# Optimization experiments

Hardware: AMD Instinct MI355X
Metric: run time of the kernel (lower is better)

The kernel has to match this reference:

```python
import jax, jax.numpy as jnp
import numpy as np

# dims: batch, n_agent, action_dim, d_model, d_inner, d_state, d_conv, delta_rank, n_block, obs_dim
B, NA, AD = 128, 8, 16
DM, DI, DS, DC, DR, NB, OD = 512, 1024, 32, 4, 32, 4, 128


def _ln(x, scale):
    m = jnp.mean(x, axis=-1, keepdims=True)
    v = jnp.var(x, axis=-1, keepdims=True)
    return (x - m) / jnp.sqrt(v + 1e-5) * scale


def _mamba_step(u, W_in, cw, cb, W_x, W_dt, b_dt, A_log, D, W_out, h, buf):
    """Single recurrent Mamba step. u:[B,DM(in)], h:[B,DI,DS], buf:[B,DC,DI]."""
    xz = u @ W_in                                   # [B, 2*DI]
    x, z = xz[:, :DI], xz[:, DI:]
    # FIFO circular buffer push (roll + write last slot)
    buf = jnp.concatenate([buf[:, 1:], x[:, None, :]], axis=1)
    # depthwise causal conv evaluated at the newest position
    xc = jax.nn.silu(jnp.einsum('bkd,kd->bd', buf, cw) + cb)
    dbc = xc @ W_x                                  # [B, DR+2*DS]
    dt, Bm, Cm = dbc[:, :DR], dbc[:, DR:DR + DS], dbc[:, DR + DS:]
    delta = jax.nn.softplus(dt @ W_dt + b_dt)       # [B, DI]
    dA = jnp.exp(delta[:, :, None] * (-jnp.exp(A_log))[None])      # [B, DI, DS]
    h = dA * h + (delta * xc)[:, :, None] * Bm[:, None, :]
    y = jnp.einsum('bds,bs->bd', h, Cm) + D * xc
    return (y * jax.nn.silu(z)) @ W_out, h, buf


def _forward(obs_rep, obs, eps, W_embed, b_embed, W_obs, ln1_s, ln2_s, ln_out, W_head, log_std,
             in_proj_s, conv_w_s, conv_b_s, x_proj_s, dt_proj_s, dt_bias_s, A_log_s, D_s, out_proj_s,
             in_proj_c, conv_w_c, conv_b_c, x_proj_c, dt_proj_c, dt_bias_c, A_log_c, D_c, out_proj_c):
    h_s = [jnp.zeros((B, DI, DS))] * NB
    h_c = [jnp.zeros((B, DI, DS))] * NB
    bf_s = [jnp.zeros((B, DC, DI))] * NB
    bf_c = [jnp.zeros((B, DC, DI))] * NB
    std = jax.nn.softplus(log_std)
    log2pi = jnp.log(2.0 * jnp.pi)
    a_prev = jnp.zeros((B, AD))                     # shifted_action[:, 0]
    acts, raws, logs = [], [], []
    for i in range(NA):
        x = a_prev @ W_embed + b_embed
        ctx = obs_rep[:, i] + obs[:, i] @ W_obs
        for b in range(NB):
            o, h_s[b], bf_s[b] = _mamba_step(_ln(x, ln1_s[b]), in_proj_s[b], conv_w_s[b], conv_b_s[b],
                                             x_proj_s[b], dt_proj_s[b], dt_bias_s[b], A_log_s[b], D_s[b],
                                             out_proj_s[b], h_s[b], bf_s[b])
            x = x + o
            o, h_c[b], bf_c[b] = _mamba_step(_ln(x, ln2_s[b]) + ctx, in_proj_c[b], conv_w_c[b], conv_b_c[b],
                                             x_proj_c[b], dt_proj_c[b], dt_bias_c[b], A_log_c[b], D_c[b],
                                             out_proj_c[b], h_c[b], bf_c[b])
            x = x + o
        mean = _ln(x, ln_out) @ W_head
        raw = mean + std * eps[:, i]                # reparameterized Normal sample
        lp = -0.5 * jnp.sum(eps[:, i] ** 2, axis=-1) - jnp.sum(jnp.log(std)) - 0.5 * AD * log2pi
        lp = lp - jnp.sum(2.0 * (jnp.log(2.0) - raw - jax.nn.softplus(-2.0 * raw)), axis=-1)
        act = jnp.tanh(raw)
        acts.append(act); raws.append(raw); logs.append(lp)
        a_prev = act                                # feed sampled action forward
    return jnp.stack(acts, 1), jnp.stack(logs, 1), jnp.stack(raws, 1)


def setup_inputs() -> dict:
    key = jax.random.key(0)
    ks = jax.random.split(key, 8)
    def rn(k, shape, s=0.02):
        return jax.random.normal(k, shape) * s
    inp = {}
    inp['obs_rep'] = jax.random.normal(ks[0], (B, NA, DM))
    inp['obs'] = jax.random.normal(ks[1], (B, NA, OD))
    inp['eps'] = jax.random.normal(ks[2], (B, NA, AD))
    inp['W_embed'] = rn(ks[3], (AD, DM))
    inp['b_embed'] = jnp.zeros((DM,))
    inp['W_obs'] = rn(ks[4], (OD, DM))
    inp['ln1_s'] = jnp.ones((NB, DM))
    inp['ln2_s'] = jnp.ones((NB, DM))
    inp['ln_out'] = jnp.ones((DM,))
    inp['W_head'] = rn(ks[5], (DM, AD))
    inp['log_std'] = jnp.zeros((AD,)) - 0.5
    def mk(kbase):
        kk = jax.random.split(kbase, 8)
        dt_u = jax.random.uniform(kk[5], (NB, DI))
        dt = jnp.clip(jnp.exp(dt_u * (jnp.log(0.1) - jnp.log(1e-3)) + jnp.log(1e-3)), 1e-4)
        dt_bias = dt + jnp.log(-jnp.expm1(-dt))     # inverse-softplus init
        return dict(
            in_proj=rn(kk[0], (NB, DM, 2 * DI)),
            conv_w=rn(kk[1], (NB, DC, DI), 0.1),
            conv_b=jnp.zeros((NB, DI)),
            x_proj=rn(kk[2], (NB, DI, DR + 2 * DS)),
            dt_proj=rn(kk[3], (NB, DR, DI), DR ** -0.5),
            dt_bias=dt_bias,
            A_log=jnp.broadcast_to(jnp.log(jnp.arange(1, DS + 1, dtype=jnp.float32)), (NB, DI, DS)) + 0.0,
            D=jnp.ones((NB, DI)),
            out_proj=rn(kk[4], (NB, DI, DM)))
    ps, pc = mk(ks[6]), mk(ks[7])
    for n, v in ps.items():
        inp[n + '_s'] = v
    for n, v in pc.items():
        inp[n + '_c'] = v
    return inp


def reference(obs_rep, obs, eps, W_embed, b_embed, W_obs, ln1_s, ln2_s, ln_out, W_head, log_std,
              in_proj_s, conv_w_s, conv_b_s, x_proj_s, dt_proj_s, dt_bias_s, A_log_s, D_s, out_proj_s,
              in_proj_c, conv_w_c, conv_b_c, x_proj_c, dt_proj_c, dt_bias_c, A_log_c, D_c, out_proj_c):
    return _forward(obs_rep, obs, eps, W_embed, b_embed, W_obs, ln1_s, ln2_s, ln_out, W_head, log_std,
                    in_proj_s, conv_w_s, conv_b_s, x_proj_s, dt_proj_s, dt_bias_s, A_log_s, D_s, out_proj_s,
                    in_proj_c, conv_w_c, conv_b_c, x_proj_c, dt_proj_c, dt_bias_c, A_log_c, D_c, out_proj_c)
```

## Files before the change

kernel.cpp:

```cpp
#include <hip/hip_runtime.h>
#include <hip/hip_bf16.h>

#define B   128
#define NA  8
#define AD  16
#define DM  512
#define DI  1024
#define DS  32
#define DC  4
#define DR  32
#define NB  4
#define OD  128

typedef unsigned int uint32;
typedef _Float16 h2f __attribute__((ext_vector_type(2)));

__device__ __forceinline__ float sigmoidf_(float x){ return 1.0f/(1.0f+__expf(-x)); }
__device__ __forceinline__ float softplusf_(float x){ return fmaxf(x,0.0f)+log1pf(__expf(-fabsf(x))); }

__device__ __forceinline__ float dot2h(uint32 a, uint32 b, float c){
    union { uint32 u; h2f h; } ua, ub;
    ua.u = a; ub.u = b;
#if __has_builtin(__builtin_amdgcn_fdot2)
    return __builtin_amdgcn_fdot2(ua.h, ub.h, c, false);
#else
    return c + (float)ua.h.x*(float)ub.h.x + (float)ua.h.y*(float)ub.h.y;
#endif
}
__device__ __forceinline__ uint32 packh2(float a, float b){
    union { uint32 u; h2f h; } w;
    w.h.x = (_Float16)a; w.h.y = (_Float16)b;
    return w.u;
}
__device__ __forceinline__ float loh(uint32 u){
    union { uint32 uu; h2f h; } w; w.uu = u; return (float)w.h.x;
}
__device__ __forceinline__ float hih(uint32 u){
    union { uint32 uu; h2f h; } w; w.uu = u; return (float)w.h.y;
}


__global__ __launch_bounds__(256) void k_negA(const float* __restrict__ Als,
    const float* __restrict__ Alc, float* __restrict__ negA)
{
    int idx = blockIdx.x*256 + threadIdx.x;
    int bs = idx >> 15;
    int r  = idx & 32767;
    int nb = bs >> 1, st = bs & 1;
    const float* src = (st ? Alc : Als) + (size_t)nb*DI*DS + r;
    negA[idx] = -__expf(*src);
}

__global__ __launch_bounds__(256) void k_ctx(const float* __restrict__ obs_rep,
    const float* __restrict__ obs, const float* __restrict__ Wobs,
    float* __restrict__ ctx)
{
    int ib = blockIdx.x;
    int b = ib >> 3, i = ib & 7;
    __shared__ float orow[OD];
    int tid = threadIdx.x;
    if (tid < OD) orow[tid] = obs[(size_t)(b*NA+i)*OD + tid];
    __syncthreads();
    for (int m = tid; m < DM; m += 256){
        float acc = obs_rep[(size_t)(b*NA+i)*DM + m];
        for (int o = 0; o < OD; o++)
            acc += orow[o]*Wobs[o*DM + m];
        ctx[(size_t)(i*B + b)*DM + m] = acc;
    }
}

__global__ __launch_bounds__(256) void k_w1h(const float* __restrict__ Ws,
    const float* __restrict__ Wc, uint32* __restrict__ W1H)
{
    int idx = blockIdx.x*256 + threadIdx.x;
    int bs = idx >> 19;
    int r  = idx & 524287;
    int k2 = r >> 11, c = r & 2047;
    int nb = bs >> 1, st = bs & 1;
    const float* src = (st ? Wc : Ws) + (size_t)nb*1048576 + (size_t)(2*k2)*2048 + c;
    W1H[idx] = packh2(src[0], src[2048]);
}

__global__ __launch_bounds__(256) void k_woh(const float* __restrict__ Ws,
    const float* __restrict__ Wc, uint32* __restrict__ WoH)
{
    int idx = blockIdx.x*256 + threadIdx.x;
    int bs = idx >> 18;
    int r  = idx & 262143;
    int k2 = r >> 9, c = r & 511;
    int nb = bs >> 1, st = bs & 1;
    const float* src = (st ? Wc : Ws) + (size_t)nb*DI*DM + (size_t)(2*k2)*DM + c;
    WoH[idx] = packh2(src[0], src[DM]);
}

__global__ __launch_bounds__(256) void k_wxh(const float* __restrict__ Ws,
    const float* __restrict__ Wc, uint32* __restrict__ WxH)
{
    int idx = blockIdx.x*256 + threadIdx.x;
    int bs = idx / 49152;
    int r  = idx % 49152;
    int j  = r >> 9, k2 = r & 511;
    int nb = bs >> 1, st = bs & 1;
    const float* src = (st ? Wc : Ws) + (size_t)nb*DI*96 + (size_t)(2*k2)*96 + j;
    WxH[idx] = packh2(src[0], src[96]);
}

__global__ __launch_bounds__(256) void k_wdth(const float* __restrict__ Ws,
    const float* __restrict__ Wc, uint32* __restrict__ WdtH)
{
    int idx = blockIdx.x*256 + threadIdx.x;
    int bs = idx >> 14;
    int r  = idx & 16383;
    int r2 = r >> 10, d = r & 1023;
    int nb = bs >> 1, st = bs & 1;
    const float* src = (st ? Wc : Ws) + (size_t)nb*DR*DI + (size_t)(2*r2)*DI + d;
    WdtH[idx] = packh2(src[0], src[DI]);
}

__global__ __launch_bounds__(256) void k_init(const float* __restrict__ bemb,
    float* __restrict__ xb0, float* __restrict__ pP)
{
    int idx = blockIdx.x*256 + threadIdx.x;
    if (idx < B*DM) xb0[idx] = bemb[idx & (DM-1)];
    pP[idx] = 0.f;
}


struct SP {
    const uint32 *W1H, *WoH, *WxH, *WdtH;
    const float *negA, *ctxG;
    const float *cw_s, *cb_s, *dtb_s, *D_s;
    const float *cw_c, *cb_c, *dtb_c, *D_c;
    const float *ln1, *ln2;
    float *xcG, *szG, *xpP, *pP;
    uint32 *convrU, *hG;
};

__global__ __launch_bounds__(1024) void k_step1(SP P, const float* __restrict__ xin,
    float* __restrict__ xout, int i, int bs)
{
    int rg = blockIdx.x >> 3, cg = blockIdx.x & 7;
    int t = threadIdx.x;
    int st = bs & 1, nb = bs >> 1;
    const float* lns = (st ? P.ln2 : P.ln1) + (size_t)nb*DM;
    const float* cw  = (st ? P.cw_c : P.cw_s) + (size_t)nb*DC*DI;
    const float* cb  = (st ? P.cb_c : P.cb_s) + (size_t)nb*DI;

    __shared__ uint32 ulnP[4][256];
    __shared__ float red1[16][4][256];
    __shared__ float xzL[4][256];
    __shared__ uint32 xcP[4][128];
    __shared__ float wred[4][2][2];
    __shared__ float ms2[4][2];

    int r = (t >> 7) & 3, cq = t & 127;
    float4 v4 = make_float4(0.f,0.f,0.f,0.f);
    if (t < 512){
        int row = rg*4 + r;
        v4 = *(const float4*)&xin[(size_t)row*DM + cq*4];
        #pragma unroll
        for (int gg = 0; gg < 8; gg++){
            float4 q4 = *(const float4*)&P.pP[((size_t)gg*B + row)*DM + cq*4];
            v4.x += q4.x; v4.y += q4.y; v4.z += q4.z; v4.w += q4.w;
        }
        if (cg == 0) *(float4*)&xout[(size_t)row*DM + cq*4] = v4;
        float sv = v4.x+v4.y+v4.z+v4.w;
        float qv = v4.x*v4.x+v4.y*v4.y+v4.z*v4.z+v4.w*v4.w;
        #pragma unroll
        for (int off = 32; off > 0; off >>= 1){
            sv += __shfl_down(sv, off);
            qv += __shfl_down(qv, off);
        }
        int lane = t & 63, wid = t >> 6;
        if (lane == 0){ wred[wid>>1][wid&1][0] = sv; wred[wid>>1][wid&1][1] = qv; }
    }
    __syncthreads();
    if (t < 4){
        float S = wred[t][0][0] + wred[t][1][0];
        float Q = wred[t][0][1] + wred[t][1][1];
        float m = S*(1.0f/DM);
        float var = Q*(1.0f/DM) - m*m;
        ms2[t][0] = m; ms2[t][1] = rsqrtf(var + 1e-5f);
    }
    __syncthreads();

    if (t < 512){
        int row = rg*4 + r;
        float m = ms2[r][0], rs = ms2[r][1];
        float4 l4 = *(const float4*)&lns[cq*4];
        float u0 = (v4.x - m)*rs*l4.x;
        float u1 = (v4.y - m)*rs*l4.y;
        float u2 = (v4.z - m)*rs*l4.z;
        float u3 = (v4.w - m)*rs*l4.w;
        if (st){
            float4 c4 = *(const float4*)&P.ctxG[((size_t)i*B + row)*DM + cq*4];
            u0 += c4.x; u1 += c4.y; u2 += c4.z; u3 += c4.w;
        }
        ulnP[r][2*cq]   = packh2(u0, u1);
        ulnP[r][2*cq+1] = packh2(u2, u3);
    }
    __syncthreads();

    {
        int cp = t & 63, kg = t >> 6;
        const uint32* w1 = P.W1H + ((size_t)bs << 19);
        int k2b = kg*16;
        const uint4* wp = (const uint4*)(w1 + ((size_t)k2b << 11)) + (cg*64 + cp);
        float a[4][4] = {};
        #pragma unroll 4
        for (int k2i = 0; k2i < 16; k2i++){
            uint4 q = wp[(size_t)k2i << 9];
            int k2 = k2b + k2i;
            uint32 u0 = ulnP[0][k2], u1 = ulnP[1][k2];
            uint32 u2 = ulnP[2][k2], u3 = ulnP[3][k2];
            a[0][0]=dot2h(u0,q.x,a[0][0]); a[0][1]=dot2h(u0,q.y,a[0][1]);
            a[0][2]=dot2h(u0,q.z,a[0][2]); a[0][3]=dot2h(u0,q.w,a[0][3]);
            a[1][0]=dot2h(u1,q.x,a[1][0]); a[1][1]=dot2h(u1,q.y,a[1][1]);
            a[1][2]=dot2h(u1,q.z,a[1][2]); a[1][3]=dot2h(u1,q.w,a[1][3]);
            a[2][0]=dot2h(u2,q.x,a[2][0]); a[2][1]=dot2h(u2,q.y,a[2][1]);
            a[2][2]=dot2h(u2,q.z,a[2][2]); a[2][3]=dot2h(u2,q.w,a[2][3]);
            a[3][0]=dot2h(u3,q.x,a[3][0]); a[3][1]=dot2h(u3,q.y,a[3][1]);
            a[3][2]=dot2h(u3,q.z,a[3][2]); a[3][3]=dot2h(u3,q.w,a[3][3]);
        }
        #pragma unroll
        for (int rr = 0; rr < 4; rr++)
            *(float4*)&red1[kg][rr][4*cp] = make_float4(a[rr][0],a[rr][1],a[rr][2],a[rr][3]);
    }
    __syncthreads();
    {
        int r2 = t >> 8, c = t & 255;
        float sacc = red1[0][r2][c];
        #pragma unroll
        for (int gk = 1; gk < 16; gk++) sacc += red1[gk][r2][c];
        xzL[r2][c] = sacc;
    }
    __syncthreads();

    if (cg < 4){
        if (t < 512){
            int r3 = r, pi = cq;
            int row3 = rg*4 + r3;
            int d0 = cg*256 + 2*pi;
            float xz0 = xzL[r3][2*pi], xz1 = xzL[r3][2*pi+1];
            uint32* ring = P.convrU + ((size_t)bs << 18);
            size_t rb = (size_t)row3*512 + (d0>>1);
            ring[((size_t)(i&3))*65536 + rb] = packh2(xz0, xz1);
            float s0 = cb[d0]   + cw[3*DI + d0]  *xz0;
            float s1 = cb[d0+1] + cw[3*DI + d0+1]*xz1;
            if (i >= 1){ uint32 uu = ring[((size_t)((i-1)&3))*65536 + rb];
                s0 += cw[2*DI + d0]*loh(uu); s1 += cw[2*DI + d0+1]*hih(uu); }
            if (i >= 2){ uint32 uu = ring[((size_t)((i-2)&3))*65536 + rb];
                s0 += cw[1*DI + d0]*loh(uu); s1 += cw[1*DI + d0+1]*hih(uu); }
            if (i >= 3){ uint32 uu = ring[((size_t)((i-3)&3))*65536 + rb];
                s0 += cw[0*DI + d0]*loh(uu); s1 += cw[0*DI + d0+1]*hih(uu); }
            float xc0 = s0*sigmoidf_(s0), xc1 = s1*sigmoidf_(s1);
            P.xcG[(size_t)row3*DI + d0]   = xc0;
            P.xcG[(size_t)row3*DI + d0+1] = xc1;
            xcP[r3][pi] = packh2(xc0, xc1);
        }
        __syncthreads();
        if (t < 384){
            int rx = t/96, j = t - rx*96;
            const uint4* wx = (const uint4*)(P.WxH + (size_t)bs*49152
                                             + ((size_t)j << 9) + (cg << 7));
            const uint32* xr = xcP[rx];
            float acc = 0.f;
            #pragma unroll 8
            for (int ii = 0; ii < 32; ii++){
                uint4 q = wx[ii];
                acc = dot2h(xr[4*ii+0], q.x, acc);
                acc = dot2h(xr[4*ii+1], q.y, acc);
                acc = dot2h(xr[4*ii+2], q.z, acc);
                acc = dot2h(xr[4*ii+3], q.w, acc);
            }
            P.xpP[((size_t)cg*B + rg*4 + rx)*96 + j] = acc;
        }
    } else {
        int r2 = t >> 8, c = t & 255;
        int row2 = rg*4 + r2;
        int d = (cg-4)*256 + c;
        float xz = xzL[r2][c];
        P.szG[(size_t)row2*DI + d] = xz*sigmoidf_(xz);
    }
}

__global__ __launch_bounds__(1024) void k_step2(SP P, int i, int bs)
{
    int rg = blockIdx.x >> 3, g = blockIdx.x & 7;
    int t = threadIdx.x;
    int st = bs & 1, nb = bs >> 1;
    const float* dtbp = (st ? P.dtb_c : P.dtb_s) + (size_t)nb*DI;
    const float* Dpp  = (st ? P.D_c   : P.D_s  ) + (size_t)nb*DI;
    const int first = (i == 0);

    __shared__ float rowS[4][96];
    __shared__ uint32 rowSP[4][16];
    __shared__ float yzL[4][128];
    __shared__ uint32 yzP[4][64];
    __shared__ float red2[8][4][624];

    if (t < 384){
        int rx = t/96, j = t - rx*96;
        int row0 = rg*4 + rx;
        size_t base = (size_t)row0*96 + j;
        rowS[rx][j] = P.xpP[base] + P.xpP[(size_t)B*96 + base]
                    + P.xpP[(size_t)2*B*96 + base] + P.xpP[(size_t)3*B*96 + base];
    }
    __syncthreads();
    if (t < 64){
        int rx = t >> 4, q = t & 15;
        rowSP[rx][q] = packh2(rowS[rx][2*q], rowS[rx][2*q+1]);
    }
    __syncthreads();

    if (t < 512){
        int r = t >> 7, dl = t & 127;
        int d = g*128 + dl;
        int row = rg*4 + r;
        float dp = dtbp[d];
        const uint32* wdt = P.WdtH + ((size_t)bs << 14) + d;
        #pragma unroll
        for (int r2 = 0; r2 < 16; r2++)
            dp = dot2h(rowSP[r][r2], wdt[(size_t)r2 << 10], dp);
        float delta = softplusf_(dp);
        float xcv = P.xcG[(size_t)row*DI + d];
        float dxc = delta*xcv;
        const float4* nap = (const float4*)(P.negA + ((size_t)bs << 15) + (size_t)d*DS);
        uint4* hb = ((uint4*)P.hG) + ((size_t)(bs*B + row) << 12) + d;
        float y = 0.f;
        #pragma unroll
        for (int qq = 0; qq < 4; qq++){
            uint4 hu = first ? make_uint4(0u,0u,0u,0u) : hb[qq << 10];
            float4 na0 = nap[2*qq], na1 = nap[2*qq+1];
            int s0 = 8*qq;
            float h0 = loh(hu.x), h1 = hih(hu.x);
            float h2 = loh(hu.y), h3 = hih(hu.y);
            float h4 = loh(hu.z), h5 = hih(hu.z);
            float h6 = loh(hu.w), h7 = hih(hu.w);
            h0 = __expf(delta*na0.x)*h0 + dxc*rowS[r][DR+s0+0];
            h1 = __expf(delta*na0.y)*h1 + dxc*rowS[r][DR+s0+1];
            h2 = __expf(delta*na0.z)*h2 + dxc*rowS[r][DR+s0+2];
            h3 = __expf(delta*na0.w)*h3 + dxc*rowS[r][DR+s0+3];
            h4 = __expf(delta*na1.x)*h4 + dxc*rowS[r][DR+s0+4];
            h5 = __expf(delta*na1.y)*h5 + dxc*rowS[r][DR+s0+5];
            h6 = __expf(delta*na1.z)*h6 + dxc*rowS[r][DR+s0+6];
            h7 = __expf(delta*na1.w)*h7 + dxc*rowS[r][DR+s0+7];
            y += h0*rowS[r][DR+DS+s0+0] + h1*rowS[r][DR+DS+s0+1]
               + h2*rowS[r][DR+DS+s0+2] + h3*rowS[r][DR+DS+s0+3]
               + h4*rowS[r][DR+DS+s0+4] + h5*rowS[r][DR+DS+s0+5]
               + h6*rowS[r][DR+DS+s0+6] + h7*rowS[r][DR+DS+s0+7];
            hu.x = packh2(h0,h1); hu.y = packh2(h2,h3);
            hu.z = packh2(h4,h5); hu.w = packh2(h6,h7);
            hb[qq << 10] = hu;
        }
        y += Dpp[d]*xcv;
        yzL[r][dl] = y*P.szG[(size_t)row*DI + d];
    }
    __syncthreads();
    if (t < 256){
        int r = t >> 6, k2 = t & 63;
        yzP[r][k2] = packh2(yzL[r][2*k2], yzL[r][2*k2+1]);
    }
    __syncthreads();

    {
        int cq = t & 127, kg = t >> 7;
        const uint32* wo = P.WoH + ((size_t)bs << 18);
        int k2b = g*64 + kg*8;
        const uint4* wp = (const uint4*)(wo + ((size_t)k2b << 9)) + cq;
        float a[4][4] = {};
        #pragma unroll
        for (int k2i = 0; k2i < 8; k2i++){
            uint4 q = wp[(size_t)k2i << 7];
            int k2l = kg*8 + k2i;
            uint32 y0 = yzP[0][k2l], y1 = yzP[1][k2l];
            uint32 y2 = yzP[2][k2l], y3 = yzP[3][k2l];
            a[0][0]=dot2h(y0,q.x,a[0][0]); a[0][1]=dot2h(y0,q.y,a[0][1]);
            a[0][2]=dot2h(y0,q.z,a[0][2]); a[0][3]=dot2h(y0,q.w,a[0][3]);
            a[1][0]=dot2h(y1,q.x,a[1][0]); a[1][1]=dot2h(y1,q.y,a[1][1]);
            a[1][2]=dot2h(y1,q.z,a[1][2]); a[1][3]=dot2h(y1,q.w,a[1][3]);
            a[2][0]=dot2h(y2,q.x,a[2][0]); a[2][1]=dot2h(y2,q.y,a[2][1]);
            a[2][2]=dot2h(y2,q.z,a[2][2]); a[2][3]=dot2h(y2,q.w,a[2][3]);
            a[3][0]=dot2h(y3,q.x,a[3][0]); a[3][1]=dot2h(y3,q.y,a[3][1]);
            a[3][2]=dot2h(y3,q.z,a[3][2]); a[3][3]=dot2h(y3,q.w,a[3][3]);
        }
        #pragma unroll
        for (int rr = 0; rr < 4; rr++)
            *(float4*)&red2[kg][rr][4*cq] = make_float4(a[rr][0],a[rr][1],a[rr][2],a[rr][3]);
    }
    __syncthreads();
    if (t < 512){
        int r2 = t >> 7, c4 = t & 127;
        float4 s = *(float4*)&red2[0][r2][4*c4];
        #pragma unroll
        for (int kg = 1; kg < 8; kg++){
            float4 q = *(float4*)&red2[kg][r2][4*c4];
            s.x += q.x; s.y += q.y; s.z += q.z; s.w += q.w;
        }
        *(float4*)&P.pP[((size_t)g*B + rg*4 + r2)*DM + 4*c4] = s;
    }
}

__global__ __launch_bounds__(512) void k_head(
    const float* __restrict__ xin, float* __restrict__ xout,
    float* __restrict__ pP,
    const float* __restrict__ lno, const float* __restrict__ Whead,
    const float* __restrict__ logstd, const float* __restrict__ eps,
    const float* __restrict__ Wemb, const float* __restrict__ bemb,
    float* __restrict__ out, int agent)
{
    int b = blockIdx.x, t = threadIdx.x, lane = t & 63, wid = t >> 6;
    __shared__ float ulnL[512];
    __shared__ float redH[512];
    __shared__ float wps[8], wpq[8], ms2[2];
    __shared__ float actv[AD], lpterm[AD];

    float v = xin[(size_t)b*DM + t];
    #pragma unroll
    for (int g = 0; g < 8; g++) v += pP[((size_t)g*B + b)*DM + t];
    float s = v, q = v*v;
    for (int off = 32; off > 0; off >>= 1){
        s += __shfl_down(s, off);
        q += __shfl_down(q, off);
    }
    if (lane == 0){ wps[wid] = s; wpq[wid] = q; }
    __syncthreads();
    if (t == 0){
        float S = 0.f, Q = 0.f;
        #pragma unroll
        for (int w2 = 0; w2 < 8; w2++){ S += wps[w2]; Q += wpq[w2]; }
        float m = S*(1.0f/DM);
        float var = Q*(1.0f/DM) - m*m;
        ms2[0] = m; ms2[1] = rsqrtf(var + 1e-5f);
    }
    __syncthreads();
    ulnL[t] = (v - ms2[0])*ms2[1]*lno[t];
    __syncthreads();
    {
        int ks = t >> 4, j = t & 15;
        float acc = 0.f;
        int k0 = ks*16;
        #pragma unroll
        for (int k = k0; k < k0 + 16; k++)
            acc += ulnL[k]*Whead[k*AD + j];
        redH[t] = acc;
    }
    __syncthreads();
    if (t < AD){
        int j = t;
        float mean = 0.f;
        #pragma unroll
        for (int ks = 0; ks < 32; ks++) mean += redH[ks*16 + j];
        float stdj = softplusf_(logstd[j]);
        float e = eps[((size_t)b*NA + agent)*AD + j];
        float raw = mean + stdj*e;
        float act = tanhf(raw);
        out[((size_t)b*NA + agent)*AD + j] = act;
        out[(size_t)NA*B*AD + (size_t)B*NA + ((size_t)b*NA + agent)*AD + j] = raw;
        actv[j] = act;
        lpterm[j] = -0.5f*e*e - logf(stdj)
                    - 2.0f*(0.69314718f - raw - softplusf_(-2.0f*raw));
    }
    __syncthreads();
    if (t == 0){
        float lp = 0.f;
        #pragma unroll
        for (int j = 0; j < AD; j++) lp += lpterm[j];
        lp -= 0.5f*AD*1.8378770664f;
        out[(size_t)NA*B*AD + (size_t)b*NA + agent] = lp;
    }
    float v2 = bemb[t];
    #pragma unroll
    for (int j = 0; j < AD; j++)
        v2 += actv[j]*Wemb[j*DM + t];
    xout[(size_t)b*DM + t] = v2;
    #pragma unroll
    for (int g = 0; g < 8; g++) pP[((size_t)g*B + b)*DM + t] = 0.f;
}


extern "C" void kernel_launch(void* const* d_in, const int* in_sizes, int n_in,
                              void* d_out, int out_size, void* d_ws, size_t ws_size,
                              hipStream_t stream)
{
    const float* in[29];
    for (int k = 0; k < 29; k++) in[k] = (const float*)d_in[k];

    char* wsb = (char*)d_ws;
    uint32* W1H  = (uint32*)(wsb + 0);
    uint32* WoH  = (uint32*)(wsb + 16777216);
    uint32* WxH  = (uint32*)(wsb + 25165824);
    uint32* WdtH = (uint32*)(wsb + 26738688);
    float*  negA = (float*) (wsb + 27262976);
    float*  ctx  = (float*) (wsb + 28311552);
    float*  xb0  = (float*) (wsb + 30408704);
    float*  xb1  = (float*) (wsb + 30670848);
    float*  xcG  = (float*) (wsb + 30932992);
    float*  szG  = (float*) (wsb + 31457280);
    float*  xpP  = (float*) (wsb + 31981568);
    float*  pP   = (float*) (wsb + 32243712);
    uint32* convrU = (uint32*)(wsb + 34340864);
    uint32* hG   = (uint32*)(wsb + 42729472);

    float* out = (float*)d_out;
    float* xb[2] = {xb0, xb1};

    k_negA<<<dim3(1024),  256, 0, stream>>>(in[17], in[26], negA);
    k_ctx <<<dim3(B*NA),  256, 0, stream>>>(in[0], in[1], in[5], ctx);
    k_w1h <<<dim3(16384), 256, 0, stream>>>(in[11], in[20], W1H);
    k_woh <<<dim3(8192),  256, 0, stream>>>(in[19], in[28], WoH);
    k_wxh <<<dim3(1536),  256, 0, stream>>>(in[14], in[23], WxH);
    k_wdth<<<dim3(512),   256, 0, stream>>>(in[15], in[24], WdtH);
    k_init<<<dim3(2048),  256, 0, stream>>>(in[4], xb0, pP);

    SP P;
    P.W1H = W1H; P.WoH = WoH; P.WxH = WxH; P.WdtH = WdtH;
    P.negA = negA; P.ctxG = ctx;
    P.cw_s = in[12]; P.cb_s = in[13]; P.dtb_s = in[16]; P.D_s = in[18];
    P.cw_c = in[21]; P.cb_c = in[22]; P.dtb_c = in[25]; P.D_c = in[27];
    P.ln1 = in[6]; P.ln2 = in[7];
    P.xcG = xcG; P.szG = szG; P.xpP = xpP; P.pP = pP;
    P.convrU = convrU; P.hG = hG;

    int cur = 0;
    for (int i = 0; i < NA; i++){
        for (int bs = 0; bs < 8; bs++){
            k_step1<<<dim3(256), 1024, 0, stream>>>(P, xb[cur], xb[cur^1], i, bs);
            cur ^= 1;
            k_step2<<<dim3(256), 1024, 0, stream>>>(P, i, bs);
        }
        k_head<<<dim3(B), 512, 0, stream>>>(xb[cur], xb[cur^1], pP,
                in[8], in[9], in[10], in[2], in[3], in[4], out, i);
        cur ^= 1;
    }
}
```

Baseline: 1.945 ms.

## Prefetch step weights into registers early, split x_proj reduction, fuse setup kernels

Loads the in_proj, out_proj and dt_proj weight slices into registers at kernel entry, so their global-memory latency overlaps the layernorm and reduction phases instead of sitting inside the dot-product loops. Splits the x_proj dot product across twice as many threads with a shared-memory partial reduction. Merges the six weight-conversion and init kernels into one launch to cut launch overhead. The register prefetch arrays raise register pressure in the 1024-thread kernels and could cause spills or lower occupancy.

```diff
diff --git a/kernel.cpp b/kernel.cpp
--- a/kernel.cpp
+++ b/kernel.cpp
@@ -40,17 +40,6 @@
 }
 
 
-__global__ __launch_bounds__(256) void k_negA(const float* __restrict__ Als,
-    const float* __restrict__ Alc, float* __restrict__ negA)
-{
-    int idx = blockIdx.x*256 + threadIdx.x;
-    int bs = idx >> 15;
-    int r  = idx & 32767;
-    int nb = bs >> 1, st = bs & 1;
-    const float* src = (st ? Alc : Als) + (size_t)nb*DI*DS + r;
-    negA[idx] = -__expf(*src);
-}
-
 __global__ __launch_bounds__(256) void k_ctx(const float* __restrict__ obs_rep,
     const float* __restrict__ obs, const float* __restrict__ Wobs,
     float* __restrict__ ctx)
@@ -69,60 +58,64 @@
     }
 }
 
-__global__ __launch_bounds__(256) void k_w1h(const float* __restrict__ Ws,
-    const float* __restrict__ Wc, uint32* __restrict__ W1H)
+__global__ __launch_bounds__(256) void k_setup(
+    const float* __restrict__ W1s, const float* __restrict__ W1c,
+    const float* __restrict__ Wos, const float* __restrict__ Woc,
+    const float* __restrict__ Wxs, const float* __restrict__ Wxc,
+    const float* __restrict__ Wds, const float* __restrict__ Wdc,
+    const float* __restrict__ Als, const float* __restrict__ Alc,
+    const float* __restrict__ bemb,
+    uint32* __restrict__ W1H, uint32* __restrict__ WoH,
+    uint32* __restrict__ WxH, uint32* __restrict__ WdtH,
+    float* __restrict__ negA, float* __restrict__ xb0, float* __restrict__ pP)
 {
     int idx = blockIdx.x*256 + threadIdx.x;
-    int bs = idx >> 19;
-    int r  = idx & 524287;
-    int k2 = r >> 11, c = r & 2047;
-    int nb = bs >> 1, st = bs & 1;
-    const float* src = (st ? Wc : Ws) + (size_t)nb*1048576 + (size_t)(2*k2)*2048 + c;
-    W1H[idx] = packh2(src[0], src[2048]);
-}
-
-__global__ __launch_bounds__(256) void k_woh(const float* __restrict__ Ws,
-    const float* __restrict__ Wc, uint32* __restrict__ WoH)
-{
-    int idx = blockIdx.x*256 + threadIdx.x;
-    int bs = idx >> 18;
-    int r  = idx & 262143;
-    int k2 = r >> 9, c = r & 511;
-    int nb = bs >> 1, st = bs & 1;
-    const float* src = (st ? Wc : Ws) + (size_t)nb*DI*DM + (size_t)(2*k2)*DM + c;
-    WoH[idx] = packh2(src[0], src[DM]);
-}
-
-__global__ __launch_bounds__(256) void k_wxh(const float* __restrict__ Ws,
-    const float* __restrict__ Wc, uint32* __restrict__ WxH)
-{
-    int idx = blockIdx.x*256 + threadIdx.x;
-    int bs = idx / 49152;
-    int r  = idx % 49152;
-    int j  = r >> 9, k2 = r & 511;
-    int nb = bs >> 1, st = bs & 1;
-    const float* src = (st ? Wc : Ws) + (size_t)nb*DI*96 + (size_t)(2*k2)*96 + j;
-    WxH[idx] = packh2(src[0], src[96]);
-}
-
-__global__ __launch_bounds__(256) void k_wdth(const float* __restrict__ Ws,
-    const float* __restrict__ Wc, uint32* __restrict__ WdtH)
-{
-    int idx = blockIdx.x*256 + threadIdx.x;
-    int bs = idx >> 14;
-    int r  = idx & 16383;
-    int r2 = r >> 10, d = r & 1023;
-    int nb = bs >> 1, st = bs & 1;
-    const float* src = (st ? Wc : Ws) + (size_t)nb*DR*DI + (size_t)(2*r2)*DI + d;
-    WdtH[idx] = packh2(src[0], src[DI]);
-}
-
-__global__ __launch_bounds__(256) void k_init(const float* __restrict__ bemb,
-    float* __restrict__ xb0, float* __restrict__ pP)
-{
-    int idx = blockIdx.x*256 + threadIdx.x;
+    if (idx < 4194304){
+        int bs = idx >> 19, rr = idx & 524287;
+        int k2 = rr >> 11, c = rr & 2047;
+        int nb = bs >> 1, st = bs & 1;
+        const float* src = (st ? W1c : W1s) + (size_t)nb*1048576 + (size_t)(2*k2)*2048 + c;
+        W1H[idx] = packh2(src[0], src[2048]);
+        return;
+    }
+    idx -= 4194304;
+    if (idx < 2097152){
+        int bs = idx >> 18, rr = idx & 262143;
+        int k2 = rr >> 9, c = rr & 511;
+        int nb = bs >> 1, st = bs & 1;
+        const float* src = (st ? Woc : Wos) + (size_t)nb*DI*DM + (size_t)(2*k2)*DM + c;
+        WoH[idx] = packh2(src[0], src[DM]);
+        return;
+    }
+    idx -= 2097152;
+    if (idx < 393216){
+        int bs = idx / 49152, rr = idx % 49152;
+        int j = rr >> 9, k2 = rr & 511;
+        int nb = bs >> 1, st = bs & 1;
+        const float* src = (st ? Wxc : Wxs) + (size_t)nb*DI*96 + (size_t)(2*k2)*96 + j;
+        WxH[idx] = packh2(src[0], src[96]);
+        return;
+    }
+    idx -= 393216;
+    if (idx < 131072){
+        int bs = idx >> 14, rr = idx & 16383;
+        int r2 = rr >> 10, d = rr & 1023;
+        int nb = bs >> 1, st = bs & 1;
+        const float* src = (st ? Wdc : Wds) + (size_t)nb*DR*DI + (size_t)(2*r2)*DI + d;
+        WdtH[idx] = packh2(src[0], src[DI]);
+        return;
+    }
+    idx -= 131072;
+    if (idx < 262144){
+        int bs = idx >> 15, rr = idx & 32767;
+        int nb = bs >> 1, st = bs & 1;
+        const float* src = (st ? Alc : Als) + (size_t)nb*DI*DS + rr;
+        negA[idx] = -__expf(*src);
+        return;
+    }
+    idx -= 262144;
+    pP[idx] = 0.f;
     if (idx < B*DM) xb0[idx] = bemb[idx & (DM-1)];
-    pP[idx] = 0.f;
 }
 
 
@@ -150,8 +143,18 @@
     __shared__ float red1[16][4][256];
     __shared__ float xzL[4][256];
     __shared__ uint32 xcP[4][128];
+    __shared__ float xpt[2][4][96];
     __shared__ float wred[4][2][2];
     __shared__ float ms2[4][2];
+
+    int cp = t & 63, kg = t >> 6;
+    uint4 wreg[16];
+    {
+        const uint32* w1 = P.W1H + ((size_t)bs << 19);
+        const uint4* wp = (const uint4*)(w1 + ((size_t)(kg*16) << 11)) + (cg*64 + cp);
+        #pragma unroll
+        for (int k2i = 0; k2i < 16; k2i++) wreg[k2i] = wp[(size_t)k2i << 9];
+    }
 
     int r = (t >> 7) & 3, cq = t & 127;
     float4 v4 = make_float4(0.f,0.f,0.f,0.f);
@@ -202,15 +205,11 @@
     __syncthreads();
 
     {
-        int cp = t & 63, kg = t >> 6;
-        const uint32* w1 = P.W1H + ((size_t)bs << 19);
-        int k2b = kg*16;
-        const uint4* wp = (const uint4*)(w1 + ((size_t)k2b << 11)) + (cg*64 + cp);
         float a[4][4] = {};
-        #pragma unroll 4
+        #pragma unroll
         for (int k2i = 0; k2i < 16; k2i++){
-            uint4 q = wp[(size_t)k2i << 9];
-            int k2 = k2b + k2i;
+            uint4 q = wreg[k2i];
+            int k2 = kg*16 + k2i;
             uint32 u0 = ulnP[0][k2], u1 = ulnP[1][k2];
             uint32 u2 = ulnP[2][k2], u3 = ulnP[3][k2];
             a[0][0]=dot2h(u0,q.x,a[0][0]); a[0][1]=dot2h(u0,q.y,a[0][1]);
@@ -259,21 +258,27 @@
             xcP[r3][pi] = packh2(xc0, xc1);
         }
         __syncthreads();
+        if (t < 768){
+            int j = t % 96, q = t / 96;
+            int rx = q & 3, ks = q >> 2;
+            const uint4* wx = (const uint4*)(P.WxH + (size_t)bs*49152
+                              + ((size_t)j << 9) + (cg << 7) + (ks << 6));
+            const uint32* xr = &xcP[rx][ks << 6];
+            float acc = 0.f;
+            #pragma unroll 8
+            for (int ii = 0; ii < 16; ii++){
+                uint4 q4 = wx[ii];
+                acc = dot2h(xr[4*ii+0], q4.x, acc);
+                acc = dot2h(xr[4*ii+1], q4.y, acc);
+                acc = dot2h(xr[4*ii+2], q4.z, acc);
+                acc = dot2h(xr[4*ii+3], q4.w, acc);
+            }
+            xpt[ks][rx][j] = acc;
+        }
+        __syncthreads();
         if (t < 384){
             int rx = t/96, j = t - rx*96;
-            const uint4* wx = (const uint4*)(P.WxH + (size_t)bs*49152
-                                             + ((size_t)j << 9) + (cg << 7));
-            const uint32* xr = xcP[rx];
-            float acc = 0.f;
-            #pragma unroll 8
-            for (int ii = 0; ii < 32; ii++){
-                uint4 q = wx[ii];
-                acc = dot2h(xr[4*ii+0], q.x, acc);
-                acc = dot2h(xr[4*ii+1], q.y, acc);
-                acc = dot2h(xr[4*ii+2], q.z, acc);
-                acc = dot2h(xr[4*ii+3], q.w, acc);
-            }
-            P.xpP[((size_t)cg*B + rg*4 + rx)*96 + j] = acc;
+            P.xpP[((size_t)cg*B + rg*4 + rx)*96 + j] = xpt[0][rx][j] + xpt[1][rx][j];
         }
     } else {
         int r2 = t >> 8, c = t & 255;
@@ -299,6 +304,23 @@
     __shared__ uint32 yzP[4][64];
     __shared__ float red2[8][4][624];
 
+    int cq = t & 127, kg = t >> 7;
+    uint4 wor[8];
+    {
+        const uint32* wo = P.WoH + ((size_t)bs << 18);
+        const uint4* wp = (const uint4*)(wo + ((size_t)(g*64 + kg*8) << 9)) + cq;
+        #pragma unroll
+        for (int k2i = 0; k2i < 8; k2i++) wor[k2i] = wp[(size_t)k2i << 7];
+    }
+    int r = (t >> 7) & 3, dl = t & 127;
+    int d = g*128 + dl;
+    uint32 wdtreg[16];
+    if (t < 512){
+        const uint32* wdt = P.WdtH + ((size_t)bs << 14) + d;
+        #pragma unroll
+        for (int r2 = 0; r2 < 16; r2++) wdtreg[r2] = wdt[(size_t)r2 << 10];
+    }
+
     if (t < 384){
         int rx = t/96, j = t - rx*96;
         int row0 = rg*4 + rx;
@@ -314,14 +336,11 @@
     __syncthreads();
 
     if (t < 512){
-        int r = t >> 7, dl = t & 127;
-        int d = g*128 + dl;
         int row = rg*4 + r;
         float dp = dtbp[d];
-        const uint32* wdt = P.WdtH + ((size_t)bs << 14) + d;
         #pragma unroll
         for (int r2 = 0; r2 < 16; r2++)
-            dp = dot2h(rowSP[r][r2], wdt[(size_t)r2 << 10], dp);
+            dp = dot2h(rowSP[r][r2], wdtreg[r2], dp);
         float delta = softplusf_(dp);
         float xcv = P.xcG[(size_t)row*DI + d];
         float dxc = delta*xcv;
@@ -358,20 +377,16 @@
     }
     __syncthreads();
     if (t < 256){
-        int r = t >> 6, k2 = t & 63;
-        yzP[r][k2] = packh2(yzL[r][2*k2], yzL[r][2*k2+1]);
+        int rr = t >> 6, k2 = t & 63;
+        yzP[rr][k2] = packh2(yzL[rr][2*k2], yzL[rr][2*k2+1]);
     }
     __syncthreads();
 
     {
-        int cq = t & 127, kg = t >> 7;
-        const uint32* wo = P.WoH + ((size_t)bs << 18);
-        int k2b = g*64 + kg*8;
-        const uint4* wp = (const uint4*)(wo + ((size_t)k2b << 9)) + cq;
         float a[4][4] = {};
         #pragma unroll
         for (int k2i = 0; k2i < 8; k2i++){
-            uint4 q = wp[(size_t)k2i << 7];
+            uint4 q = wor[k2i];
             int k2l = kg*8 + k2i;
             uint32 y0 = yzP[0][k2l], y1 = yzP[1][k2l];
             uint32 y2 = yzP[2][k2l], y3 = yzP[3][k2l];
@@ -393,8 +408,8 @@
         int r2 = t >> 7, c4 = t & 127;
         float4 s = *(float4*)&red2[0][r2][4*c4];
         #pragma unroll
-        for (int kg = 1; kg < 8; kg++){
-            float4 q = *(float4*)&red2[kg][r2][4*c4];
+        for (int kk = 1; kk < 8; kk++){
+            float4 q = *(float4*)&red2[kk][r2][4*c4];
             s.x += q.x; s.y += q.y; s.z += q.z; s.w += q.w;
         }
         *(float4*)&P.pP[((size_t)g*B + rg*4 + r2)*DM + 4*c4] = s;
@@ -505,13 +520,10 @@
     float* out = (float*)d_out;
     float* xb[2] = {xb0, xb1};
 
-    k_negA<<<dim3(1024),  256, 0, stream>>>(in[17], in[26], negA);
-    k_ctx <<<dim3(B*NA),  256, 0, stream>>>(in[0], in[1], in[5], ctx);
-    k_w1h <<<dim3(16384), 256, 0, stream>>>(in[11], in[20], W1H);
-    k_woh <<<dim3(8192),  256, 0, stream>>>(in[19], in[28], WoH);
-    k_wxh <<<dim3(1536),  256, 0, stream>>>(in[14], in[23], WxH);
-    k_wdth<<<dim3(512),   256, 0, stream>>>(in[15], in[24], WdtH);
-    k_init<<<dim3(2048),  256, 0, stream>>>(in[4], xb0, pP);
+    k_setup<<<dim3(29696), 256, 0, stream>>>(
+        in[11], in[20], in[19], in[28], in[14], in[23], in[15], in[24],
+        in[17], in[26], in[4], W1H, WoH, WxH, WdtH, negA, xb0, pP);
+    k_ctx<<<dim3(B*NA), 256, 0, stream>>>(in[0], in[1], in[5], ctx);
 
     SP P;
     P.W1H = W1H; P.WoH = WoH; P.WxH = WxH; P.WdtH = WdtH;
```

New measurement: 2.021 ms. 3.9% more time.
